# Kernel optimization log

Measured on AMD Instinct MI355X. Metric: run time of the kernel, lower is better.

Reference implementation:

```python
import jax, jax.numpy as jnp
import numpy as np

DIM = 768
HEADS = 12
HEAD_DIM = DIM // HEADS
SCALE = DIM ** (-0.5)  # NOTE: module scales by full dim, not head_dim


def setup_inputs() -> dict:
    key = jax.random.key(0)
    k1, k2, k3 = jax.random.split(key, 3)
    B, N = 4, 2048
    x = jax.random.normal(k1, (B, N, DIM), dtype=jnp.float32)
    W_qkv = jax.random.normal(k2, (DIM, 3 * DIM), dtype=jnp.float32) * (DIM ** -0.5)
    W_proj = jax.random.normal(k3, (DIM, DIM), dtype=jnp.float32) * (DIM ** -0.5)
    b_proj = jnp.zeros((DIM,), dtype=jnp.float32)
    return {"x": x, "W_qkv": W_qkv, "W_proj": W_proj, "b_proj": b_proj}


def reference(x, W_qkv, W_proj, b_proj):
    B, N, C = x.shape
    qkv = x @ W_qkv  # [B, N, 3C]
    qkv = qkv.reshape(B, N, 3, HEADS, HEAD_DIM)
    qkv = jnp.transpose(qkv, (2, 0, 3, 1, 4))  # [3, B, H, N, hd]
    q, k, v = qkv[0], qkv[1], qkv[2]
    att = jnp.einsum('bhnd,bhmd->bhnm', q, k) * SCALE
    att = jax.nn.softmax(att, axis=-1)
    # drop=0.0 -> dropout is identity
    out = jnp.einsum('bhnm,bhmd->bhnd', att, v)  # [B, H, N, hd]
    out = jnp.transpose(out, (0, 2, 1, 3)).reshape(B, N, C)
    return out @ W_proj + b_proj
```

## Files before the change

### kernel.cpp

```cpp
#include <hip/hip_runtime.h>
#include <hip/hip_bf16.h>

#define HEADS 12
#define HD    64
#define SEQ   2048
#define CDIM  768
#define QKV_SCALE 0.03608439182435161f
#define LOG2E 1.4426950408889634f
#define SM_C (QKV_SCALE * LOG2E)

typedef __attribute__((ext_vector_type(8))) short bf16x8;
typedef __attribute__((ext_vector_type(4))) float f32x4;
typedef __attribute__((ext_vector_type(4))) unsigned short usx4;
typedef __attribute__((ext_vector_type(8))) unsigned short usx8;
typedef __attribute__((ext_vector_type(2))) unsigned int uix2;
typedef __attribute__((ext_vector_type(4))) unsigned int uix4;

__device__ __forceinline__ unsigned short f2bf(float f) {
  union { __hip_bfloat16 h; unsigned short u; } c;
  c.h = __float2bfloat16(f);
  return c.u;
}

__device__ __forceinline__ float exp2_fast(float x) {
  float r; asm("v_exp_f32 %0, %1" : "=v"(r) : "v"(x)); return r;
}

__device__ __forceinline__ unsigned int cvt_pk_bf16(float lo, float hi) {
  unsigned int r; asm("v_cvt_pk_bf16_f32 %0, %1, %2" : "=v"(r) : "v"(lo), "v"(hi)); return r;
}

__device__ __forceinline__ void gload_lds16(const unsigned short* g, unsigned short* l) {
  __builtin_amdgcn_global_load_lds(
      (__attribute__((address_space(1))) void*)(g),
      (__attribute__((address_space(3))) void*)(l), 16, 0, 0);
}

__global__ __launch_bounds__(256) void k_prep(
    const float* __restrict__ x, unsigned short* __restrict__ xb,
    const float* __restrict__ Wqkv, unsigned short* __restrict__ WqkvT,
    const float* __restrict__ Wproj, unsigned short* __restrict__ WprojT) {
  __shared__ float tile[32][33];
  const int b = blockIdx.x;
  if (b < 3072) {
    int i = b * 256 + threadIdx.x;
    const float4* s4 = (const float4*)x;
    float4 a = s4[i * 2 + 0];
    float4 d = s4[i * 2 + 1];
    usx8 r;
    r[0] = f2bf(a.x); r[1] = f2bf(a.y); r[2] = f2bf(a.z); r[3] = f2bf(a.w);
    r[4] = f2bf(d.x); r[5] = f2bf(d.y); r[6] = f2bf(d.z); r[7] = f2bf(d.w);
    *(usx8*)&xb[i * 8] = r;
    return;
  }
  const float* src; unsigned short* dst; int C, c0, k0;
  if (b < 4800) {
    int tb = b - 3072;
    src = Wqkv; dst = WqkvT; C = 2304;
    c0 = (tb % 72) * 32; k0 = (tb / 72) * 32;
  } else {
    int tb = b - 4800;
    src = Wproj; dst = WprojT; C = 768;
    c0 = (tb % 24) * 32; k0 = (tb / 24) * 32;
  }
  int tx = threadIdx.x & 31;
  int ty = threadIdx.x >> 5;
#pragma unroll
  for (int i = 0; i < 32; i += 8)
    tile[ty + i][tx] = src[(size_t)(k0 + ty + i) * C + c0 + tx];
  __syncthreads();
#pragma unroll
  for (int i = 0; i < 32; i += 8)
    dst[(size_t)(c0 + ty + i) * 768 + k0 + tx] = f2bf(tile[tx][ty + i]);
}

__global__ __launch_bounds__(256) void k_qkv_gemm(
    const unsigned short* __restrict__ A,
    const unsigned short* __restrict__ Bt,
    unsigned short* __restrict__ Qb, unsigned short* __restrict__ Kb,
    unsigned short* __restrict__ Vt) {
  __shared__ unsigned short As[128 * 64];
  __shared__ unsigned short Bs[128 * 64];
  const int lane = threadIdx.x & 63, w = threadIdx.x >> 6;
  const int wm = w >> 1, wn = w & 1;
  const int id = blockIdx.y * 18 + blockIdx.x;
  const int lin = (id & 7) * 144 + (id >> 3);
  const int r0 = (lin / 18) * 128, c0 = (lin % 18) * 128;
  f32x4 acc[4][4] = {};

  for (int k0 = 0; k0 < 768; k0 += 64) {
#pragma unroll
    for (int iss = 0; iss < 4; ++iss) {
      int eo = (w * 4 + iss) * 512 + lane * 8;
      int row = eo >> 6;
      int cc = ((eo >> 3) & 7) ^ (row & 7);
      gload_lds16(A + (size_t)(r0 + row) * 768 + k0 + cc * 8, &As[(w * 4 + iss) * 512]);
    }
#pragma unroll
    for (int iss = 0; iss < 4; ++iss) {
      int eo = (w * 4 + iss) * 512 + lane * 8;
      int row = eo >> 6;
      int cc = ((eo >> 3) & 7) ^ (row & 7);
      gload_lds16(Bt + (size_t)(c0 + row) * 768 + k0 + cc * 8, &Bs[(w * 4 + iss) * 512]);
    }
    asm volatile("s_waitcnt vmcnt(0)" ::: "memory");
    __syncthreads();

#pragma unroll
    for (int ks = 0; ks < 2; ++ks) {
      bf16x8 af[4], bfr[4];
#pragma unroll
      for (int f = 0; f < 4; ++f) {
        int ar = wm * 64 + f * 16 + (lane & 15);
        int ac = (ks * 4 + (lane >> 4)) ^ (ar & 7);
        af[f] = *(const bf16x8*)&As[ar * 64 + ac * 8];
        int br = wn * 64 + f * 16 + (lane & 15);
        int bc = (ks * 4 + (lane >> 4)) ^ (br & 7);
        bfr[f] = *(const bf16x8*)&Bs[br * 64 + bc * 8];
      }
#pragma unroll
      for (int fm = 0; fm < 4; ++fm)
#pragma unroll
        for (int fn = 0; fn < 4; ++fn)
          acc[fm][fn] = __builtin_amdgcn_mfma_f32_16x16x32_bf16(af[fm], bfr[fn], acc[fm][fn], 0, 0, 0);
    }
    __syncthreads();
  }

  const int which = c0 / 768;
  const float qsc = (which == 0) ? SM_C : 1.0f;
#pragma unroll
  for (int fm = 0; fm < 4; ++fm) {
    int gr0 = r0 + wm * 64 + fm * 16 + ((lane >> 4) << 2);
    int bb = gr0 >> 11, n0 = gr0 & 2047;
#pragma unroll
    for (int fn = 0; fn < 4; ++fn) {
      int gc = c0 + wn * 64 + fn * 16 + (lane & 15);
      int rem = gc - which * 768;
      int h = rem >> 6, d = rem & 63;
      int bh = bb * HEADS + h;
      f32x4 v = acc[fm][fn];
      if (which == 2) {
        usx4 p;
        p[0] = f2bf(v[0]); p[1] = f2bf(v[1]); p[2] = f2bf(v[2]); p[3] = f2bf(v[3]);
        *(usx4*)&Vt[(size_t)(bh * 64 + d) * 2048 + n0] = p;
      } else {
        unsigned short* dst = (which == 0 ? Qb : Kb) + (size_t)(bh * 2048 + n0) * 64 + d;
        dst[0]   = f2bf(v[0] * qsc);
        dst[64]  = f2bf(v[1] * qsc);
        dst[128] = f2bf(v[2] * qsc);
        dst[192] = f2bf(v[3] * qsc);
      }
    }
  }
}

__global__ __launch_bounds__(256, 2) void k_attn(
    const unsigned short* __restrict__ Qb, const unsigned short* __restrict__ Kb,
    const unsigned short* __restrict__ Vt, unsigned short* __restrict__ Ob) {
  __shared__ unsigned short Ksm[2][64 * 64];
  __shared__ unsigned short Vsm[2][64 * 64];
  const int lane = threadIdx.x & 63, w = threadIdx.x >> 6;
  const int g = lane >> 4, c = lane & 15;

  int id = blockIdx.x + (blockIdx.y << 4);
  int lin = (id & 7) * 96 + (id >> 3);
  int bx = lin & 15, bh = lin >> 4;
  const int q0 = bx * 128 + w * 32;
  const int bb = bh / HEADS, h = bh % HEADS;

  const unsigned short* Qp = Qb + (size_t)bh * SEQ * HD;
  const unsigned short* Kp = Kb + (size_t)bh * SEQ * HD;
  const unsigned short* Vp = Vt + (size_t)bh * HD * SEQ;

  bf16x8 aQ[2][2];
#pragma unroll
  for (int qf = 0; qf < 2; ++qf)
#pragma unroll
    for (int ks = 0; ks < 2; ++ks)
      aQ[qf][ks] = *(const bf16x8*)&Qp[(size_t)(q0 + qf * 16 + c) * 64 + ks * 32 + g * 8];

  float lrun[2] = {0.f, 0.f};
  f32x4 accOT[4][2] = {};
  const f32x4 fzero = {0.f, 0.f, 0.f, 0.f};

  int offf[2][4];
#pragma unroll
  for (int ks = 0; ks < 2; ++ks)
#pragma unroll
    for (int f = 0; f < 4; ++f) {
      int row = f * 16 + c;
      offf[ks][f] = row * 64 + (((ks * 4 + g) ^ (row & 7)) * 8);
    }

  const int eo0 = (w * 2 + 0) * 512 + lane * 8;
  const int row0 = eo0 >> 6, cc0 = ((eo0 >> 3) & 7) ^ (row0 & 7);
  const int eo1 = (w * 2 + 1) * 512 + lane * 8;
  const int row1 = eo1 >> 6, cc1 = ((eo1 >> 3) & 7) ^ (row1 & 7);
  const unsigned short* kga = Kp + (size_t)row0 * 64 + cc0 * 8;
  const unsigned short* kgb = Kp + (size_t)row1 * 64 + cc1 * 8;
  const unsigned short* vga = Vp + (size_t)row0 * 2048 + cc0 * 8;
  const unsigned short* vgb = Vp + (size_t)row1 * 2048 + cc1 * 8;

  gload_lds16(kga, &Ksm[0][(w * 2 + 0) * 512]);
  gload_lds16(kgb, &Ksm[0][(w * 2 + 1) * 512]);
  gload_lds16(vga, &Vsm[0][(w * 2 + 0) * 512]);
  gload_lds16(vgb, &Vsm[0][(w * 2 + 1) * 512]);
  asm volatile("s_waitcnt vmcnt(0)" ::: "memory");
  __syncthreads();

  auto TILE = [&](int t, int buf) {
    if (t + 1 < 32) {
      gload_lds16(kga + (t + 1) * 4096, &Ksm[buf ^ 1][(w * 2 + 0) * 512]);
      gload_lds16(kgb + (t + 1) * 4096, &Ksm[buf ^ 1][(w * 2 + 1) * 512]);
      gload_lds16(vga + (t + 1) * 64,   &Vsm[buf ^ 1][(w * 2 + 0) * 512]);
      gload_lds16(vgb + (t + 1) * 64,   &Vsm[buf ^ 1][(w * 2 + 1) * 512]);
    }

    bf16x8 kf0[4], kf1[4];
#pragma unroll
    for (int fm = 0; fm < 4; ++fm) {
      kf0[fm] = *(const bf16x8*)&Ksm[buf][offf[0][fm]];
      kf1[fm] = *(const bf16x8*)&Ksm[buf][offf[1][fm]];
    }
    f32x4 st[4][2];
    __builtin_amdgcn_s_setprio(1);
#pragma unroll
    for (int fm = 0; fm < 4; ++fm)
#pragma unroll
      for (int qf = 0; qf < 2; ++qf)
        st[fm][qf] = __builtin_amdgcn_mfma_f32_16x16x32_bf16(kf0[fm], aQ[qf][0], fzero, 0, 0, 0);
#pragma unroll
    for (int fm = 0; fm < 4; ++fm)
#pragma unroll
      for (int qf = 0; qf < 2; ++qf)
        st[fm][qf] = __builtin_amdgcn_mfma_f32_16x16x32_bf16(kf1[fm], aQ[qf][1], st[fm][qf], 0, 0, 0);
    __builtin_amdgcn_s_setprio(0);

    uix4 pfrag[2][2];
#pragma unroll
    for (int qf = 0; qf < 2; ++qf) {
      float p[4][4];
      float ts[4];
#pragma unroll
      for (int fm = 0; fm < 4; ++fm) {
        p[fm][0] = exp2_fast(st[fm][qf][0]);
        p[fm][1] = exp2_fast(st[fm][qf][1]);
        p[fm][2] = exp2_fast(st[fm][qf][2]);
        p[fm][3] = exp2_fast(st[fm][qf][3]);
        ts[fm] = (p[fm][0] + p[fm][1]) + (p[fm][2] + p[fm][3]);
      }
      lrun[qf] += (ts[0] + ts[1]) + (ts[2] + ts[3]);

#pragma unroll
      for (int ks = 0; ks < 2; ++ks)
#pragma unroll
        for (int tt = 0; tt < 2; ++tt) {
          unsigned int a = cvt_pk_bf16(p[2 * ks][2 * tt], p[2 * ks][2 * tt + 1]);
          unsigned int b = cvt_pk_bf16(p[2 * ks + 1][2 * tt], p[2 * ks + 1][2 * tt + 1]);
          uix2 s1 = __builtin_amdgcn_permlane32_swap(a, b, false, false);
          uix2 s2 = __builtin_amdgcn_permlane16_swap(s1[0], s1[1], false, false);
          pfrag[ks][qf][tt] = s2[0];
          pfrag[ks][qf][2 + tt] = s2[1];
        }
    }

    bf16x8 vf0[4], vf1[4];
#pragma unroll
    for (int fd = 0; fd < 4; ++fd) {
      vf0[fd] = *(const bf16x8*)&Vsm[buf][offf[0][fd]];
      vf1[fd] = *(const bf16x8*)&Vsm[buf][offf[1][fd]];
    }
    __builtin_amdgcn_s_setprio(1);
#pragma unroll
    for (int fd = 0; fd < 4; ++fd)
#pragma unroll
      for (int qf = 0; qf < 2; ++qf) {
        accOT[fd][qf] = __builtin_amdgcn_mfma_f32_16x16x32_bf16(
            vf0[fd], *(const bf16x8*)&pfrag[0][qf], accOT[fd][qf], 0, 0, 0);
        accOT[fd][qf] = __builtin_amdgcn_mfma_f32_16x16x32_bf16(
            vf1[fd], *(const bf16x8*)&pfrag[1][qf], accOT[fd][qf], 0, 0, 0);
      }
    __builtin_amdgcn_s_setprio(0);

    asm volatile("s_waitcnt vmcnt(0)" ::: "memory");
    __syncthreads();
  };

  for (int kt = 0; kt < 32; kt += 2) {
    TILE(kt, 0);
    TILE(kt + 1, 1);
  }

#pragma unroll
  for (int qf = 0; qf < 2; ++qf) {
    float l = lrun[qf];
    l += __shfl_xor(l, 16);
    l += __shfl_xor(l, 32);
    float rl = 1.0f / l;
    int n = q0 + qf * 16 + c;
#pragma unroll
    for (int fd = 0; fd < 4; ++fd) {
      f32x4 v = accOT[fd][qf];
      usx4 pk;
      pk[0] = f2bf(v[0] * rl); pk[1] = f2bf(v[1] * rl);
      pk[2] = f2bf(v[2] * rl); pk[3] = f2bf(v[3] * rl);
      *(usx4*)&Ob[(size_t)(bb * SEQ + n) * CDIM + h * HD + fd * 16 + 4 * g] = pk;
    }
  }
}

__global__ __launch_bounds__(256) void k_proj_gemm(
    const unsigned short* __restrict__ A,
    const unsigned short* __restrict__ Bt,
    const float* __restrict__ bias, float* __restrict__ out) {
  __shared__ unsigned short As[64 * 64];
  __shared__ unsigned short Bs[128 * 64];
  const int lane = threadIdx.x & 63, w = threadIdx.x >> 6;
  const int wm = w & 1, wn = w >> 1;
  const int id = blockIdx.y * 6 + blockIdx.x;
  const int lin = (id & 7) * 96 + (id >> 3);
  const int r0 = (lin / 6) * 64, c0 = (lin % 6) * 128;
  f32x4 acc[2][4] = {};

  for (int k0 = 0; k0 < 768; k0 += 64) {
#pragma unroll
    for (int iss = 0; iss < 2; ++iss) {
      int eo = (w * 2 + iss) * 512 + lane * 8;
      int row = eo >> 6;
      int cc = ((eo >> 3) & 7) ^ (row & 7);
      gload_lds16(A + (size_t)(r0 + row) * 768 + k0 + cc * 8, &As[(w * 2 + iss) * 512]);
    }
#pragma unroll
    for (int iss = 0; iss < 4; ++iss) {
      int eo = (w * 4 + iss) * 512 + lane * 8;
      int row = eo >> 6;
      int cc = ((eo >> 3) & 7) ^ (row & 7);
      gload_lds16(Bt + (size_t)(c0 + row) * 768 + k0 + cc * 8, &Bs[(w * 4 + iss) * 512]);
    }
    asm volatile("s_waitcnt vmcnt(0)" ::: "memory");
    __syncthreads();

#pragma unroll
    for (int ks = 0; ks < 2; ++ks) {
      bf16x8 af[2], bfr[4];
#pragma unroll
      for (int f = 0; f < 2; ++f) {
        int ar = wm * 32 + f * 16 + (lane & 15);
        int ac = (ks * 4 + (lane >> 4)) ^ (ar & 7);
        af[f] = *(const bf16x8*)&As[ar * 64 + ac * 8];
      }
#pragma unroll
      for (int f = 0; f < 4; ++f) {
        int br = wn * 64 + f * 16 + (lane & 15);
        int bc = (ks * 4 + (lane >> 4)) ^ (br & 7);
        bfr[f] = *(const bf16x8*)&Bs[br * 64 + bc * 8];
      }
#pragma unroll
      for (int fm = 0; fm < 2; ++fm)
#pragma unroll
        for (int fn = 0; fn < 4; ++fn)
          acc[fm][fn] = __builtin_amdgcn_mfma_f32_16x16x32_bf16(af[fm], bfr[fn], acc[fm][fn], 0, 0, 0);
    }
    __syncthreads();
  }

#pragma unroll
  for (int fm = 0; fm < 2; ++fm) {
    int gr0 = r0 + wm * 32 + fm * 16 + ((lane >> 4) << 2);
#pragma unroll
    for (int fn = 0; fn < 4; ++fn) {
      int gc = c0 + wn * 64 + fn * 16 + (lane & 15);
      float bsv = bias[gc];
      f32x4 v = acc[fm][fn];
#pragma unroll
      for (int r = 0; r < 4; ++r)
        out[(size_t)(gr0 + r) * CDIM + gc] = v[r] + bsv;
    }
  }
}

extern "C" void kernel_launch(void* const* d_in, const int* in_sizes, int n_in,
                              void* d_out, int out_size, void* d_ws, size_t ws_size,
                              hipStream_t stream) {
  const float* x      = (const float*)d_in[0];
  const float* W_qkv  = (const float*)d_in[1];
  const float* W_proj = (const float*)d_in[2];
  const float* b_proj = (const float*)d_in[3];
  float* out = (float*)d_out;

  unsigned short* ws     = (unsigned short*)d_ws;
  unsigned short* xb     = ws;
  unsigned short* WqkvT  = xb + 6291456;
  unsigned short* WprojT = WqkvT + 1769472;
  unsigned short* Qb     = WprojT + 589824;
  unsigned short* Kb     = Qb + 6291456;
  unsigned short* Vt     = Kb + 6291456;
  unsigned short* Ob     = Vt + 6291456;

  k_prep<<<5376, 256, 0, stream>>>(x, xb, W_qkv, WqkvT, W_proj, WprojT);
  k_qkv_gemm<<<dim3(18, 64), 256, 0, stream>>>(xb, WqkvT, Qb, Kb, Vt);
  k_attn<<<dim3(16, 48), 256, 0, stream>>>(Qb, Kb, Vt, Ob);
  k_proj_gemm<<<dim3(6, 128), 256, 0, stream>>>(Ob, WprojT, b_proj, out);
}
```

Baseline: 136.8 us.

## Double-buffer LDS tiles in QKV and projection GEMMs to overlap loads with MFMA

Both GEMM kernels now keep two LDS buffers per operand and issue the global-to-LDS loads for the next K tile before running the MFMAs on the current one. A single wait and barrier sits at the end of each step instead of before the compute. Per-thread global address bases are also precomputed once. This is meant to hide global load latency behind matrix math, at the cost of doubling LDS use (64KB for the QKV kernel), which may lower occupancy.

```diff
diff --git a/kernel.cpp b/kernel.cpp
--- a/kernel.cpp
+++ b/kernel.cpp
@@ -79,8 +79,8 @@
     const unsigned short* __restrict__ Bt,
     unsigned short* __restrict__ Qb, unsigned short* __restrict__ Kb,
     unsigned short* __restrict__ Vt) {
-  __shared__ unsigned short As[128 * 64];
-  __shared__ unsigned short Bs[128 * 64];
+  __shared__ unsigned short As[2][128 * 64];
+  __shared__ unsigned short Bs[2][128 * 64];
   const int lane = threadIdx.x & 63, w = threadIdx.x >> 6;
   const int wm = w >> 1, wn = w & 1;
   const int id = blockIdx.y * 18 + blockIdx.x;
@@ -88,24 +88,30 @@
   const int r0 = (lin / 18) * 128, c0 = (lin % 18) * 128;
   f32x4 acc[4][4] = {};
 
-  for (int k0 = 0; k0 < 768; k0 += 64) {
+  const unsigned short* aptr[4];
+  const unsigned short* bptr[4];
+#pragma unroll
+  for (int iss = 0; iss < 4; ++iss) {
+    int e = (w * 4 + iss) * 512 + lane * 8;
+    int row = e >> 6, cc = ((e >> 3) & 7) ^ (row & 7);
+    aptr[iss] = A  + (size_t)(r0 + row) * 768 + cc * 8;
+    bptr[iss] = Bt + (size_t)(c0 + row) * 768 + cc * 8;
+  }
+
+  auto STAGE = [&](int k0, int b) {
 #pragma unroll
     for (int iss = 0; iss < 4; ++iss) {
-      int eo = (w * 4 + iss) * 512 + lane * 8;
-      int row = eo >> 6;
-      int cc = ((eo >> 3) & 7) ^ (row & 7);
-      gload_lds16(A + (size_t)(r0 + row) * 768 + k0 + cc * 8, &As[(w * 4 + iss) * 512]);
-    }
-#pragma unroll
-    for (int iss = 0; iss < 4; ++iss) {
-      int eo = (w * 4 + iss) * 512 + lane * 8;
-      int row = eo >> 6;
-      int cc = ((eo >> 3) & 7) ^ (row & 7);
-      gload_lds16(Bt + (size_t)(c0 + row) * 768 + k0 + cc * 8, &Bs[(w * 4 + iss) * 512]);
-    }
-    asm volatile("s_waitcnt vmcnt(0)" ::: "memory");
-    __syncthreads();
-
+      gload_lds16(aptr[iss] + k0, &As[b][(w * 4 + iss) * 512]);
+      gload_lds16(bptr[iss] + k0, &Bs[b][(w * 4 + iss) * 512]);
+    }
+  };
+
+  STAGE(0, 0);
+  asm volatile("s_waitcnt vmcnt(0)" ::: "memory");
+  __syncthreads();
+
+  auto KSTEP = [&](int t, int buf) {
+    if (t + 1 < 12) STAGE((t + 1) * 64, buf ^ 1);
 #pragma unroll
     for (int ks = 0; ks < 2; ++ks) {
       bf16x8 af[4], bfr[4];
@@ -113,10 +119,10 @@
       for (int f = 0; f < 4; ++f) {
         int ar = wm * 64 + f * 16 + (lane & 15);
         int ac = (ks * 4 + (lane >> 4)) ^ (ar & 7);
-        af[f] = *(const bf16x8*)&As[ar * 64 + ac * 8];
+        af[f] = *(const bf16x8*)&As[buf][ar * 64 + ac * 8];
         int br = wn * 64 + f * 16 + (lane & 15);
         int bc = (ks * 4 + (lane >> 4)) ^ (br & 7);
-        bfr[f] = *(const bf16x8*)&Bs[br * 64 + bc * 8];
+        bfr[f] = *(const bf16x8*)&Bs[buf][br * 64 + bc * 8];
       }
 #pragma unroll
       for (int fm = 0; fm < 4; ++fm)
@@ -124,7 +130,13 @@
         for (int fn = 0; fn < 4; ++fn)
           acc[fm][fn] = __builtin_amdgcn_mfma_f32_16x16x32_bf16(af[fm], bfr[fn], acc[fm][fn], 0, 0, 0);
     }
+    asm volatile("s_waitcnt vmcnt(0)" ::: "memory");
     __syncthreads();
+  };
+
+  for (int t = 0; t < 12; t += 2) {
+    KSTEP(t, 0);
+    KSTEP(t + 1, 1);
   }
 
   const int which = c0 / 768;
@@ -314,8 +326,8 @@
     const unsigned short* __restrict__ A,
     const unsigned short* __restrict__ Bt,
     const float* __restrict__ bias, float* __restrict__ out) {
-  __shared__ unsigned short As[64 * 64];
-  __shared__ unsigned short Bs[128 * 64];
+  __shared__ unsigned short As[2][64 * 64];
+  __shared__ unsigned short Bs[2][128 * 64];
   const int lane = threadIdx.x & 63, w = threadIdx.x >> 6;
   const int wm = w & 1, wn = w >> 1;
   const int id = blockIdx.y * 6 + blockIdx.x;
@@ -323,24 +335,36 @@
   const int r0 = (lin / 6) * 64, c0 = (lin % 6) * 128;
   f32x4 acc[2][4] = {};
 
-  for (int k0 = 0; k0 < 768; k0 += 64) {
-#pragma unroll
-    for (int iss = 0; iss < 2; ++iss) {
-      int eo = (w * 2 + iss) * 512 + lane * 8;
-      int row = eo >> 6;
-      int cc = ((eo >> 3) & 7) ^ (row & 7);
-      gload_lds16(A + (size_t)(r0 + row) * 768 + k0 + cc * 8, &As[(w * 2 + iss) * 512]);
-    }
-#pragma unroll
-    for (int iss = 0; iss < 4; ++iss) {
-      int eo = (w * 4 + iss) * 512 + lane * 8;
-      int row = eo >> 6;
-      int cc = ((eo >> 3) & 7) ^ (row & 7);
-      gload_lds16(Bt + (size_t)(c0 + row) * 768 + k0 + cc * 8, &Bs[(w * 4 + iss) * 512]);
-    }
-    asm volatile("s_waitcnt vmcnt(0)" ::: "memory");
-    __syncthreads();
-
+  const unsigned short* aptr[2];
+  const unsigned short* bptr[4];
+#pragma unroll
+  for (int iss = 0; iss < 2; ++iss) {
+    int e = (w * 2 + iss) * 512 + lane * 8;
+    int row = e >> 6, cc = ((e >> 3) & 7) ^ (row & 7);
+    aptr[iss] = A + (size_t)(r0 + row) * 768 + cc * 8;
+  }
+#pragma unroll
+  for (int iss = 0; iss < 4; ++iss) {
+    int e = (w * 4 + iss) * 512 + lane * 8;
+    int row = e >> 6, cc = ((e >> 3) & 7) ^ (row & 7);
+    bptr[iss] = Bt + (size_t)(c0 + row) * 768 + cc * 8;
+  }
+
+  auto STAGE = [&](int k0, int b) {
+#pragma unroll
+    for (int iss = 0; iss < 2; ++iss)
+      gload_lds16(aptr[iss] + k0, &As[b][(w * 2 + iss) * 512]);
+#pragma unroll
+    for (int iss = 0; iss < 4; ++iss)
+      gload_lds16(bptr[iss] + k0, &Bs[b][(w * 4 + iss) * 512]);
+  };
+
+  STAGE(0, 0);
+  asm volatile("s_waitcnt vmcnt(0)" ::: "memory");
+  __syncthreads();
+
+  auto KSTEP = [&](int t, int buf) {
+    if (t + 1 < 12) STAGE((t + 1) * 64, buf ^ 1);
 #pragma unroll
     for (int ks = 0; ks < 2; ++ks) {
       bf16x8 af[2], bfr[4];
@@ -348,13 +372,13 @@
       for (int f = 0; f < 2; ++f) {
         int ar = wm * 32 + f * 16 + (lane & 15);
         int ac = (ks * 4 + (lane >> 4)) ^ (ar & 7);
-        af[f] = *(const bf16x8*)&As[ar * 64 + ac * 8];
+        af[f] = *(const bf16x8*)&As[buf][ar * 64 + ac * 8];
       }
 #pragma unroll
       for (int f = 0; f < 4; ++f) {
         int br = wn * 64 + f * 16 + (lane & 15);
         int bc = (ks * 4 + (lane >> 4)) ^ (br & 7);
-        bfr[f] = *(const bf16x8*)&Bs[br * 64 + bc * 8];
+        bfr[f] = *(const bf16x8*)&Bs[buf][br * 64 + bc * 8];
       }
 #pragma unroll
       for (int fm = 0; fm < 2; ++fm)
@@ -362,7 +386,13 @@
         for (int fn = 0; fn < 4; ++fn)
           acc[fm][fn] = __builtin_amdgcn_mfma_f32_16x16x32_bf16(af[fm], bfr[fn], acc[fm][fn], 0, 0, 0);
     }
+    asm volatile("s_waitcnt vmcnt(0)" ::: "memory");
     __syncthreads();
+  };
+
+  for (int t = 0; t < 12; t += 2) {
+    KSTEP(t, 0);
+    KSTEP(t + 1, 1);
   }
 
 #pragma unroll
```

After: 137.2 us. No clear change (+0.3%).
